# Performance work log

Hardware: AMD Instinct MI355X
Metric: run time of the kernel (lower is better)

Reference implementation:

```python
import jax, jax.numpy as jnp
import numpy as np

NUM_EXPERTS = 8
HIDDEN = 1024
FFN = 2048
TOKENS = 2048


def setup_inputs() -> dict:
    key = jax.random.key(0)
    k_x, k_idx, k_w1, k_w2 = jax.random.split(key, 4)
    scale = 0.02
    x = jax.random.normal(k_x, (TOKENS, HIDDEN), dtype=jnp.float32)
    expert_indices = jax.random.randint(k_idx, (TOKENS,), 0, NUM_EXPERTS, dtype=jnp.int64)
    W1 = jax.random.normal(k_w1, (NUM_EXPERTS, HIDDEN, FFN), dtype=jnp.float32) * scale
    b1 = jnp.zeros((NUM_EXPERTS, FFN), dtype=jnp.float32)
    W2 = jax.random.normal(k_w2, (NUM_EXPERTS, FFN, HIDDEN), dtype=jnp.float32) * scale
    b2 = jnp.zeros((NUM_EXPERTS, HIDDEN), dtype=jnp.float32)
    return {"x": x, "expert_indices": expert_indices, "W1": W1, "b1": b1, "W2": W2, "b2": b2}


def reference(x, expert_indices, W1, b1, W2, b2):
    # Each token routed to one expert's MLP: Linear -> GELU(exact) -> Linear.
    # Dropout is identity in eval mode. Loop is over the small fixed expert set.
    out = jnp.zeros_like(x)
    for e in range(NUM_EXPERTS):
        h = jax.nn.gelu(x @ W1[e] + b1[e], approximate=False)  # [T, FFN]
        y = h @ W2[e] + b2[e]                                   # [T, H]
        mask = (expert_indices == e)[:, None]
        out = out + jnp.where(mask, y, 0.0)
    return out
```

## Files before the change

kernel.cpp:

```cpp
#include <hip/hip_runtime.h>

#define T_TOK 2048
#define HID   1024
#define FFN   2048
#define NEXP  8
#define MAX_SLOTS 24

typedef __attribute__((ext_vector_type(8))) short bf16x8;
typedef __attribute__((ext_vector_type(4))) float f32x4;

__device__ __forceinline__ short f2bf(float f) {
    unsigned u = __builtin_bit_cast(unsigned, f);
    u = (u + 0x7fffu + ((u >> 16) & 1u)) >> 16;
    return (short)u;
}

__device__ __forceinline__ float gelu_exact(float x) {
    return 0.5f * x * (1.0f + erff(x * 0.70710678118654752f));
}

__device__ __forceinline__ void async_cp16(const short* g, short* l) {
    __builtin_amdgcn_global_load_lds(
        (const __attribute__((address_space(1))) unsigned int*)g,
        (__attribute__((address_space(3))) unsigned int*)l, 16, 0, 0);
}

__device__ __forceinline__ void wtrans_body(
        const float* __restrict__ W, short* __restrict__ WT,
        int K, int N, int e, int kblk, int nblk) {
    int tid = threadIdx.x;
    int w = tid >> 6, l = tid & 63;
    int kb = kblk * 32 + w * 8;
    int n4 = nblk * 256 + l * 4;
    const float* src = W + (size_t)e * K * N + (size_t)kb * N + n4;
    float4 v[8];
#pragma unroll
    for (int r = 0; r < 8; r++)
        v[r] = *(const float4*)(src + (size_t)r * N);
    int kpanel = kb >> 6;
    int kc = (kb >> 3) & 7;
    int npanel = n4 >> 7;
    int n_in = n4 & 127;
    int kpanels = K >> 6;
    short* dst = WT + (size_t)e * K * N
               + ((size_t)npanel * kpanels + kpanel) * 8192
               + kc * 1024 + n_in * 8;
#pragma unroll
    for (int j = 0; j < 4; j++) {
        bf16x8 o = {f2bf(((const float*)&v[0])[j]), f2bf(((const float*)&v[1])[j]),
                    f2bf(((const float*)&v[2])[j]), f2bf(((const float*)&v[3])[j]),
                    f2bf(((const float*)&v[4])[j]), f2bf(((const float*)&v[5])[j]),
                    f2bf(((const float*)&v[6])[j]), f2bf(((const float*)&v[7])[j])};
        *(bf16x8*)(dst + j * 8) = o;
    }
}

__global__ __launch_bounds__(256) void prep_kernel(
        const float* __restrict__ x, const int* __restrict__ idx,
        const float* __restrict__ W1, const float* __restrict__ W2,
        short* __restrict__ xb,
        short* __restrict__ W1T, short* __restrict__ W2T,
        int* __restrict__ offs, int* __restrict__ cnts,
        int* __restrict__ tokl,
        int* __restrict__ slot_e, int* __restrict__ slot_t0) {
    int bx = blockIdx.x;
    int tid = threadIdx.x;
    if (bx < 2048) {
        int e = bx >> 8, rem = bx & 255;
        wtrans_body(W1, W1T, HID, FFN, e, rem & 31, rem >> 5);
    } else if (bx < 4096) {
        int b = bx - 2048;
        int e = b >> 8, rem = b & 255;
        wtrans_body(W2, W2T, FFN, HID, e, rem & 63, rem >> 6);
    } else if (bx < 5120) {
        int i = ((bx - 4096) * 256 + tid) * 8;
        float4 v0 = *(const float4*)(x + i);
        float4 v1 = *(const float4*)(x + i + 4);
        bf16x8 r = {f2bf(v0.x), f2bf(v0.y), f2bf(v0.z), f2bf(v0.w),
                    f2bf(v1.x), f2bf(v1.y), f2bf(v1.z), f2bf(v1.w)};
        *(bf16x8*)(xb + i) = r;
    } else {
        __shared__ int c[NEXP], cur[NEXP], o[NEXP];
        if (tid < NEXP) { c[tid] = 0; cur[tid] = 0; }
        __syncthreads();
        for (int t = tid; t < T_TOK; t += 256) atomicAdd(&c[idx[t]], 1);
        __syncthreads();
        if (tid == 0) {
            int s = 0;
            for (int e = 0; e < NEXP; e++) { o[e] = s; s += c[e]; }
            int ns = 0;
            for (int e = 0; e < NEXP; e++)
                for (int t0 = 0; t0 < c[e]; t0 += 128) {
                    slot_e[ns] = e; slot_t0[ns] = t0; ns++;
                }
            for (; ns < MAX_SLOTS; ns++) slot_e[ns] = -1;
        }
        __syncthreads();
        if (tid < NEXP) { offs[tid] = o[tid]; cnts[tid] = c[tid]; }
        for (int t = tid; t < T_TOK; t += 256) {
            int e = idx[t];
            int p = o[e] + atomicAdd(&cur[e], 1);
            tokl[p] = t;
        }
    }
}

__global__ __launch_bounds__(256) void gemm1_kernel(
        const short* __restrict__ xb, const short* __restrict__ W1T,
        const float* __restrict__ b1,
        const int* __restrict__ offs, const int* __restrict__ cnts,
        const int* __restrict__ tokl,
        const int* __restrict__ slot_e, const int* __restrict__ slot_t0,
        short* __restrict__ hg) {
    int s = blockIdx.y;
    int e = slot_e[s];
    if (e < 0) return;
    int t0 = slot_t0[s], count = cnts[e], off = offs[e];
    int n0 = blockIdx.x * 128;

    __shared__ short As[128 * 64];
    __shared__ short Bs[8 * 128 * 8];
    __shared__ int stok[128];

    int tid = threadIdx.x;
    if (tid < 128) {
        int p = t0 + tid;
        stok[tid] = tokl[off + (p < count ? p : count - 1)];
    }
    __syncthreads();

    int w = tid >> 6, l = tid & 63, l15 = l & 15, quad = l >> 4;
    int wm = (w >> 1) * 64, wn = (w & 1) * 64;
    int lsub = l >> 3, cs = l & 7;

    const short* gA[4];
    short* lA[4];
#pragma unroll
    for (int i = 0; i < 4; i++) {
        int m = w * 32 + i * 8 + lsub;
        int c = (cs - m) & 7;
        gA[i] = xb + (size_t)stok[m] * HID + c * 8;
        lA[i] = As + w * 2048 + i * 512 + l * 8;
    }

    const short* Bpan = W1T + (size_t)e * (HID * FFN)
                      + (size_t)(n0 >> 7) * ((HID >> 6) * 8192);
    int bo[4];
#pragma unroll
    for (int i = 0; i < 4; i++) bo[i] = (w * 4 + i) * 512 + l * 8;

    f32x4 acc[4][4];
#pragma unroll
    for (int i = 0; i < 4; i++)
#pragma unroll
        for (int j = 0; j < 4; j++) acc[i][j] = (f32x4){0.f, 0.f, 0.f, 0.f};

    for (int kt = 0; kt < HID / 64; kt++) {
        const short* bp = Bpan + (size_t)kt * 8192;
#pragma unroll
        for (int i = 0; i < 4; i++) async_cp16(gA[i], lA[i]);
#pragma unroll
        for (int i = 0; i < 4; i++) async_cp16(bp + bo[i], Bs + bo[i]);
#pragma unroll
        for (int i = 0; i < 4; i++) gA[i] += 64;
        __syncthreads();
#pragma unroll
        for (int kk = 0; kk < 2; kk++) {
            bf16x8 a[4], b[4];
#pragma unroll
            for (int mt = 0; mt < 4; mt++) {
                int m = wm + mt * 16 + l15;
                a[mt] = *(const bf16x8*)&As[m * 64 + (((kk * 4 + quad) + m) & 7) * 8];
            }
#pragma unroll
            for (int nt = 0; nt < 4; nt++) {
                int n = wn + nt * 16 + l15;
                b[nt] = *(const bf16x8*)&Bs[(kk * 4 + quad) * 1024 + n * 8];
            }
#pragma unroll
            for (int mt = 0; mt < 4; mt++)
#pragma unroll
                for (int nt = 0; nt < 4; nt++)
                    acc[mt][nt] = __builtin_amdgcn_mfma_f32_16x16x32_bf16(
                        a[mt], b[nt], acc[mt][nt], 0, 0, 0);
        }
        __syncthreads();
    }

    const float* b1e = b1 + e * FFN + n0;
#pragma unroll
    for (int mt = 0; mt < 4; mt++) {
        int rbase = wm + mt * 16 + quad * 4;
#pragma unroll
        for (int nt = 0; nt < 4; nt++) {
            int coln = wn + nt * 16 + l15;
            float bb = b1e[coln];
#pragma unroll
            for (int r = 0; r < 4; r++) {
                int p = t0 + rbase + r;
                if (p < count)
                    hg[(size_t)(off + p) * FFN + n0 + coln] =
                        f2bf(gelu_exact(acc[mt][nt][r] + bb));
            }
        }
    }
}

__global__ __launch_bounds__(256) void gemm2_kernel(
        const short* __restrict__ hg, const short* __restrict__ W2T,
        const float* __restrict__ b2,
        const int* __restrict__ offs, const int* __restrict__ cnts,
        const int* __restrict__ tokl,
        const int* __restrict__ slot_e, const int* __restrict__ slot_t0,
        float* __restrict__ out) {
    int s = blockIdx.y;
    int e = slot_e[s];
    if (e < 0) return;
    int t0 = slot_t0[s], count = cnts[e], off = offs[e];
    int n0 = blockIdx.x * 128;

    __shared__ short As[128 * 64];
    __shared__ short Bs[8 * 128 * 8];
    __shared__ int stok[128];

    int tid = threadIdx.x;
    if (tid < 128) {
        int p = t0 + tid;
        stok[tid] = tokl[off + (p < count ? p : count - 1)];
    }
    __syncthreads();

    int w = tid >> 6, l = tid & 63, l15 = l & 15, quad = l >> 4;
    int wm = (w >> 1) * 64, wn = (w & 1) * 64;
    int lsub = l >> 3, cs = l & 7;

    const short* gA[4];
    short* lA[4];
#pragma unroll
    for (int i = 0; i < 4; i++) {
        int m = w * 32 + i * 8 + lsub;
        int c = (cs - m) & 7;
        int gm = off + (t0 + m < count ? t0 + m : count - 1);
        gA[i] = hg + (size_t)gm * FFN + c * 8;
        lA[i] = As + w * 2048 + i * 512 + l * 8;
    }

    const short* Bpan = W2T + (size_t)e * (FFN * HID)
                      + (size_t)(n0 >> 7) * ((FFN >> 6) * 8192);
    int bo[4];
#pragma unroll
    for (int i = 0; i < 4; i++) bo[i] = (w * 4 + i) * 512 + l * 8;

    f32x4 acc[4][4];
#pragma unroll
    for (int i = 0; i < 4; i++)
#pragma unroll
        for (int j = 0; j < 4; j++) acc[i][j] = (f32x4){0.f, 0.f, 0.f, 0.f};

    for (int kt = 0; kt < FFN / 64; kt++) {
        const short* bp = Bpan + (size_t)kt * 8192;
#pragma unroll
        for (int i = 0; i < 4; i++) async_cp16(gA[i], lA[i]);
#pragma unroll
        for (int i = 0; i < 4; i++) async_cp16(bp + bo[i], Bs + bo[i]);
#pragma unroll
        for (int i = 0; i < 4; i++) gA[i] += 64;
        __syncthreads();
#pragma unroll
        for (int kk = 0; kk < 2; kk++) {
            bf16x8 a[4], b[4];
#pragma unroll
            for (int mt = 0; mt < 4; mt++) {
                int m = wm + mt * 16 + l15;
                a[mt] = *(const bf16x8*)&As[m * 64 + (((kk * 4 + quad) + m) & 7) * 8];
            }
#pragma unroll
            for (int nt = 0; nt < 4; nt++) {
                int n = wn + nt * 16 + l15;
                b[nt] = *(const bf16x8*)&Bs[(kk * 4 + quad) * 1024 + n * 8];
            }
#pragma unroll
            for (int mt = 0; mt < 4; mt++)
#pragma unroll
                for (int nt = 0; nt < 4; nt++)
                    acc[mt][nt] = __builtin_amdgcn_mfma_f32_16x16x32_bf16(
                        a[mt], b[nt], acc[mt][nt], 0, 0, 0);
        }
        __syncthreads();
    }

    const float* b2e = b2 + e * HID + n0;
#pragma unroll
    for (int mt = 0; mt < 4; mt++) {
        int rbase = wm + mt * 16 + quad * 4;
#pragma unroll
        for (int nt = 0; nt < 4; nt++) {
            int coln = wn + nt * 16 + l15;
            float bb = b2e[coln];
#pragma unroll
            for (int r = 0; r < 4; r++) {
                int p = t0 + rbase + r;
                if (p < count) {
                    int tok = stok[rbase + r];
                    out[(size_t)tok * HID + n0 + coln] = acc[mt][nt][r] + bb;
                }
            }
        }
    }
}

extern "C" void kernel_launch(void* const* d_in, const int* in_sizes, int n_in,
                              void* d_out, int out_size, void* d_ws, size_t ws_size,
                              hipStream_t stream) {
    const float* x   = (const float*)d_in[0];
    const int*   idx = (const int*)d_in[1];
    const float* W1  = (const float*)d_in[2];
    const float* b1  = (const float*)d_in[3];
    const float* W2  = (const float*)d_in[4];
    const float* b2  = (const float*)d_in[5];
    float* out = (float*)d_out;

    const size_t META = 32768;
    int*   offs    = (int*)d_ws;
    int*   cnts    = offs + 8;
    int*   tokl    = offs + 16;
    int*   slot_e  = offs + 16 + T_TOK;
    int*   slot_t0 = slot_e + MAX_SLOTS;
    char*  base    = (char*)d_ws + META;
    short* xb  = (short*)base;
    short* hg  = (short*)(base + (size_t)T_TOK * HID * 2);
    short* W1T = (short*)(base + (size_t)T_TOK * HID * 2 + (size_t)T_TOK * FFN * 2);
    short* W2T = W1T + (size_t)NEXP * FFN * HID;

    prep_kernel<<<5121, 256, 0, stream>>>(
        x, idx, W1, W2, xb, W1T, W2T,
        offs, cnts, tokl, slot_e, slot_t0);

    gemm1_kernel<<<dim3(FFN / 128, MAX_SLOTS), 256, 0, stream>>>(
        xb, W1T, b1, offs, cnts, tokl, slot_e, slot_t0, hg);
    gemm2_kernel<<<dim3(HID / 128, MAX_SLOTS), 256, 0, stream>>>(
        hg, W2T, b2, offs, cnts, tokl, slot_e, slot_t0, out);
}
```

Measured before the change: 244.1 us.

## Double-buffer GEMM tiles and split-K the second GEMM with atomic accumulation

Both GEMM kernels now use two LDS buffers, so the next K-tile's async global-to-LDS copy is issued before the current tile's MFMA work. This is meant to hide load latency behind compute. The second GEMM is split along K into two halves via a third grid dimension, which doubles its block count to improve CU occupancy. Its results are accumulated with fp32 atomicAdd into an output that the prep kernel now pre-fills with the per-expert b2 bias. The shared token-index staging is replaced by direct tokl reads. In exchange, LDS use per block doubles, atomic traffic is added on the output, and summation order becomes nondeterministic.

```diff
diff --git a/kernel.cpp b/kernel.cpp
--- a/kernel.cpp
+++ b/kernel.cpp
@@ -57,8 +57,9 @@
 
 __global__ __launch_bounds__(256) void prep_kernel(
         const float* __restrict__ x, const int* __restrict__ idx,
+        const float* __restrict__ b2,
         const float* __restrict__ W1, const float* __restrict__ W2,
-        short* __restrict__ xb,
+        short* __restrict__ xb, float* __restrict__ out,
         short* __restrict__ W1T, short* __restrict__ W2T,
         int* __restrict__ offs, int* __restrict__ cnts,
         int* __restrict__ tokl,
@@ -79,6 +80,11 @@
         bf16x8 r = {f2bf(v0.x), f2bf(v0.y), f2bf(v0.z), f2bf(v0.w),
                     f2bf(v1.x), f2bf(v1.y), f2bf(v1.z), f2bf(v1.w)};
         *(bf16x8*)(xb + i) = r;
+    } else if (bx < 7168) {
+        int t = bx - 5120;
+        int e = idx[t];
+        ((float4*)(out + (size_t)t * HID))[tid] =
+            ((const float4*)(b2 + (size_t)e * HID))[tid];
     } else {
         __shared__ int c[NEXP], cur[NEXP], o[NEXP];
         if (tid < NEXP) { c[tid] = 0; cur[tid] = 0; }
@@ -118,29 +124,24 @@
     int t0 = slot_t0[s], count = cnts[e], off = offs[e];
     int n0 = blockIdx.x * 128;
 
-    __shared__ short As[128 * 64];
-    __shared__ short Bs[8 * 128 * 8];
-    __shared__ int stok[128];
+    __shared__ short As[2 * 128 * 64];
+    __shared__ short Bs[2 * 8 * 128 * 8];
 
     int tid = threadIdx.x;
-    if (tid < 128) {
-        int p = t0 + tid;
-        stok[tid] = tokl[off + (p < count ? p : count - 1)];
-    }
-    __syncthreads();
-
     int w = tid >> 6, l = tid & 63, l15 = l & 15, quad = l >> 4;
     int wm = (w >> 1) * 64, wn = (w & 1) * 64;
     int lsub = l >> 3, cs = l & 7;
 
     const short* gA[4];
-    short* lA[4];
+    int lAoff[4];
 #pragma unroll
     for (int i = 0; i < 4; i++) {
         int m = w * 32 + i * 8 + lsub;
         int c = (cs - m) & 7;
-        gA[i] = xb + (size_t)stok[m] * HID + c * 8;
-        lA[i] = As + w * 2048 + i * 512 + l * 8;
+        int p = t0 + m;
+        int tok = tokl[off + (p < count ? p : count - 1)];
+        gA[i] = xb + (size_t)tok * HID + c * 8;
+        lAoff[i] = w * 2048 + i * 512 + l * 8;
     }
 
     const short* Bpan = W1T + (size_t)e * (HID * FFN)
@@ -149,33 +150,44 @@
 #pragma unroll
     for (int i = 0; i < 4; i++) bo[i] = (w * 4 + i) * 512 + l * 8;
 
+    auto stage = [&](int buf, int kt) {
+        const short* bp = Bpan + (size_t)kt * 8192;
+        short* As_b = As + buf * 8192;
+        short* Bs_b = Bs + buf * 8192;
+#pragma unroll
+        for (int i = 0; i < 4; i++) async_cp16(gA[i], As_b + lAoff[i]);
+#pragma unroll
+        for (int i = 0; i < 4; i++) async_cp16(bp + bo[i], Bs_b + bo[i]);
+#pragma unroll
+        for (int i = 0; i < 4; i++) gA[i] += 64;
+    };
+
     f32x4 acc[4][4];
 #pragma unroll
     for (int i = 0; i < 4; i++)
 #pragma unroll
         for (int j = 0; j < 4; j++) acc[i][j] = (f32x4){0.f, 0.f, 0.f, 0.f};
 
-    for (int kt = 0; kt < HID / 64; kt++) {
-        const short* bp = Bpan + (size_t)kt * 8192;
-#pragma unroll
-        for (int i = 0; i < 4; i++) async_cp16(gA[i], lA[i]);
-#pragma unroll
-        for (int i = 0; i < 4; i++) async_cp16(bp + bo[i], Bs + bo[i]);
-#pragma unroll
-        for (int i = 0; i < 4; i++) gA[i] += 64;
-        __syncthreads();
+    stage(0, 0);
+    __syncthreads();
+
+    const int KT = HID / 64;
+    for (int kt = 0; kt < KT; kt++) {
+        if (kt + 1 < KT) stage((kt + 1) & 1, kt + 1);
+        const short* As_b = As + (kt & 1) * 8192;
+        const short* Bs_b = Bs + (kt & 1) * 8192;
 #pragma unroll
         for (int kk = 0; kk < 2; kk++) {
             bf16x8 a[4], b[4];
 #pragma unroll
             for (int mt = 0; mt < 4; mt++) {
                 int m = wm + mt * 16 + l15;
-                a[mt] = *(const bf16x8*)&As[m * 64 + (((kk * 4 + quad) + m) & 7) * 8];
+                a[mt] = *(const bf16x8*)&As_b[m * 64 + (((kk * 4 + quad) + m) & 7) * 8];
             }
 #pragma unroll
             for (int nt = 0; nt < 4; nt++) {
                 int n = wn + nt * 16 + l15;
-                b[nt] = *(const bf16x8*)&Bs[(kk * 4 + quad) * 1024 + n * 8];
+                b[nt] = *(const bf16x8*)&Bs_b[(kk * 4 + quad) * 1024 + n * 8];
             }
 #pragma unroll
             for (int mt = 0; mt < 4; mt++)
@@ -208,7 +220,6 @@
 
 __global__ __launch_bounds__(256) void gemm2_kernel(
         const short* __restrict__ hg, const short* __restrict__ W2T,
-        const float* __restrict__ b2,
         const int* __restrict__ offs, const int* __restrict__ cnts,
         const int* __restrict__ tokl,
         const int* __restrict__ slot_e, const int* __restrict__ slot_t0,
@@ -217,67 +228,73 @@
     int e = slot_e[s];
     if (e < 0) return;
     int t0 = slot_t0[s], count = cnts[e], off = offs[e];
+    int ks = blockIdx.z;
     int n0 = blockIdx.x * 128;
 
-    __shared__ short As[128 * 64];
-    __shared__ short Bs[8 * 128 * 8];
-    __shared__ int stok[128];
+    __shared__ short As[2 * 128 * 64];
+    __shared__ short Bs[2 * 8 * 128 * 8];
 
     int tid = threadIdx.x;
-    if (tid < 128) {
-        int p = t0 + tid;
-        stok[tid] = tokl[off + (p < count ? p : count - 1)];
-    }
-    __syncthreads();
-
     int w = tid >> 6, l = tid & 63, l15 = l & 15, quad = l >> 4;
     int wm = (w >> 1) * 64, wn = (w & 1) * 64;
     int lsub = l >> 3, cs = l & 7;
 
     const short* gA[4];
-    short* lA[4];
+    int lAoff[4];
 #pragma unroll
     for (int i = 0; i < 4; i++) {
         int m = w * 32 + i * 8 + lsub;
         int c = (cs - m) & 7;
         int gm = off + (t0 + m < count ? t0 + m : count - 1);
-        gA[i] = hg + (size_t)gm * FFN + c * 8;
-        lA[i] = As + w * 2048 + i * 512 + l * 8;
+        gA[i] = hg + (size_t)gm * FFN + ks * 1024 + c * 8;
+        lAoff[i] = w * 2048 + i * 512 + l * 8;
     }
 
     const short* Bpan = W2T + (size_t)e * (FFN * HID)
-                      + (size_t)(n0 >> 7) * ((FFN >> 6) * 8192);
+                      + (size_t)(n0 >> 7) * ((FFN >> 6) * 8192)
+                      + (size_t)ks * 16 * 8192;
     int bo[4];
 #pragma unroll
     for (int i = 0; i < 4; i++) bo[i] = (w * 4 + i) * 512 + l * 8;
 
+    auto stage = [&](int buf, int kt) {
+        const short* bp = Bpan + (size_t)kt * 8192;
+        short* As_b = As + buf * 8192;
+        short* Bs_b = Bs + buf * 8192;
+#pragma unroll
+        for (int i = 0; i < 4; i++) async_cp16(gA[i], As_b + lAoff[i]);
+#pragma unroll
+        for (int i = 0; i < 4; i++) async_cp16(bp + bo[i], Bs_b + bo[i]);
+#pragma unroll
+        for (int i = 0; i < 4; i++) gA[i] += 64;
+    };
+
     f32x4 acc[4][4];
 #pragma unroll
     for (int i = 0; i < 4; i++)
 #pragma unroll
         for (int j = 0; j < 4; j++) acc[i][j] = (f32x4){0.f, 0.f, 0.f, 0.f};
 
-    for (int kt = 0; kt < FFN / 64; kt++) {
-        const short* bp = Bpan + (size_t)kt * 8192;
-#pragma unroll
-        for (int i = 0; i < 4; i++) async_cp16(gA[i], lA[i]);
-#pragma unroll
-        for (int i = 0; i < 4; i++) async_cp16(bp + bo[i], Bs + bo[i]);
-#pragma unroll
-        for (int i = 0; i < 4; i++) gA[i] += 64;
-        __syncthreads();
+    stage(0, 0);
+    __syncthreads();
+
+    const int KT = 16;
+    for (int kt = 0; kt < KT; kt++) {
+        if (kt + 1 < KT) stage((kt + 1) & 1, kt + 1);
+        const short* As_b = As + (kt & 1) * 8192;
+        const short* Bs_b = Bs + (kt & 1) * 8192;
 #pragma unroll
         for (int kk = 0; kk < 2; kk++) {
             bf16x8 a[4], b[4];
 #pragma unroll
             for (int mt = 0; mt < 4; mt++) {
                 int m = wm + mt * 16 + l15;
-                a[mt] = *(const bf16x8*)&As[m * 64 + (((kk * 4 + quad) + m) & 7) * 8];
+                a[mt] = *(const bf16x8*)&As_b[m * 64 + (((kk * 4 + quad) + m) & 7) * 8];
             }
 #pragma unroll
             for (int nt = 0; nt < 4; nt++) {
                 int n = wn + nt * 16 + l15;
-                b[nt] = *(const bf16x8*)&Bs[(kk * 4 + quad) * 1024 + n * 8];
+                b[nt] = *(const bf16x8*)&Bs_b[(kk * 4 + quad) * 1024 + n * 8];
             }
 #pragma unroll
             for (int mt = 0; mt < 4; mt++)
@@ -289,20 +306,18 @@
         __syncthreads();
     }
 
-    const float* b2e = b2 + e * HID + n0;
 #pragma unroll
     for (int mt = 0; mt < 4; mt++) {
         int rbase = wm + mt * 16 + quad * 4;
 #pragma unroll
         for (int nt = 0; nt < 4; nt++) {
-            int coln = wn + nt * 16 + l15;
-            float bb = b2e[coln];
+            int coln = n0 + wn + nt * 16 + l15;
 #pragma unroll
             for (int r = 0; r < 4; r++) {
                 int p = t0 + rbase + r;
                 if (p < count) {
-                    int tok = stok[rbase + r];
-                    out[(size_t)tok * HID + n0 + coln] = acc[mt][nt][r] + bb;
+                    int tok = tokl[off + p];
+                    atomicAdd(out + (size_t)tok * HID + coln, acc[mt][nt][r]);
                 }
             }
         }
@@ -332,12 +347,12 @@
     short* W1T = (short*)(base + (size_t)T_TOK * HID * 2 + (size_t)T_TOK * FFN * 2);
     short* W2T = W1T + (size_t)NEXP * FFN * HID;
 
-    prep_kernel<<<5121, 256, 0, stream>>>(
-        x, idx, W1, W2, xb, W1T, W2T,
+    prep_kernel<<<7169, 256, 0, stream>>>(
+        x, idx, b2, W1, W2, xb, out, W1T, W2T,
         offs, cnts, tokl, slot_e, slot_t0);
 
     gemm1_kernel<<<dim3(FFN / 128, MAX_SLOTS), 256, 0, stream>>>(
         xb, W1T, b1, offs, cnts, tokl, slot_e, slot_t0, hg);
-    gemm2_kernel<<<dim3(HID / 128, MAX_SLOTS), 256, 0, stream>>>(
-        hg, W2T, b2, offs, cnts, tokl, slot_e, slot_t0, out);
-}
+    gemm2_kernel<<<dim3(HID / 128, MAX_SLOTS, 2), 256, 0, stream>>>(
+        hg, W2T, offs, cnts, tokl, slot_e, slot_t0, out);
+}
```

Result: slower. 259.0 us (+6.1%).
